# Performance work log

Measured on AMD Instinct MI355X. Metric: run time of the kernel, lower is better.

## Reference

```python
import math
import jax
import jax.numpy as jnp
import numpy as np

IMAGE_SIZE = 256
FOV_DEG = 60.0
NEAR, FAR = 0.01, 10.0
CHUNK = 128          # faces processed per scan step (bounds peak memory)
BIG_Z = 1e10         # 'infinite' depth for empty pixels


def _projection_matrix():
    f = 1.0 / math.tan(math.radians(FOV_DEG) / 2)
    return jnp.array([
        [f, 0.0, 0.0, 0.0],
        [0.0, f, 0.0, 0.0],
        [0.0, 0.0, (FAR + NEAR) / (NEAR - FAR), 2.0 * FAR * NEAR / (NEAR - FAR)],
        [0.0, 0.0, -1.0, 0.0],
    ], dtype=jnp.float32)


def _rasterize_mask(v_ndc, faces):
    """Coverage mask via edge-function triangle rasterization with a z-buffer.
    v_ndc: [V,3] ndc coords, faces: [F,3] int. Returns float [H,W] mask."""
    H = W = IMAGE_SIZE
    dt = v_ndc.dtype
    px = ((jnp.arange(W, dtype=dt) + 0.5) / W * 2.0 - 1.0)[None, None, :]  # [1,1,W]
    py = ((jnp.arange(H, dtype=dt) + 0.5) / H * 2.0 - 1.0)[None, :, None]  # [1,H,1]
    fchunks = faces.reshape(-1, CHUNK, 3)

    def body(carry, fc):
        zbuf, mask = carry
        tri = v_ndc[fc]  # [C,3,3]
        x0 = tri[:, 0, 0][:, None, None]; y0 = tri[:, 0, 1][:, None, None]; z0 = tri[:, 0, 2][:, None, None]
        x1 = tri[:, 1, 0][:, None, None]; y1 = tri[:, 1, 1][:, None, None]; z1 = tri[:, 1, 2][:, None, None]
        x2 = tri[:, 2, 0][:, None, None]; y2 = tri[:, 2, 1][:, None, None]; z2 = tri[:, 2, 2][:, None, None]
        # edge functions, [C,H,W]
        e0 = (x1 - x0) * (py - y0) - (y1 - y0) * (px - x0)
        e1 = (x2 - x1) * (py - y1) - (y2 - y1) * (px - x1)
        e2 = (x0 - x2) * (py - y2) - (y0 - y2) * (px - x2)
        inside = ((e0 >= 0) & (e1 >= 0) & (e2 >= 0)) | ((e0 <= 0) & (e1 <= 0) & (e2 <= 0))
        area = e0 + e1 + e2
        denom = jnp.where(jnp.abs(area) > 1e-12, area, 1.0)
        # barycentric-interpolated depth
        z = (e1 * z0 + e2 * z1 + e0 * z2) / denom
        zc = jnp.where(inside, z, BIG_Z)
        zbuf = jnp.minimum(zbuf, jnp.min(zc, axis=0))
        mask = jnp.maximum(mask, jnp.max(inside.astype(dt), axis=0))
        return (zbuf, mask), None

    zbuf0 = jnp.full((H, W), BIG_Z, dtype=dt)
    mask0 = jnp.zeros((H, W), dtype=dt)
    (_, mask), _ = jax.lax.scan(body, (zbuf0, mask0), fchunks)
    return mask


def setup_inputs() -> dict:
    key = jax.random.key(0)
    k1, k2, k3, k4 = jax.random.split(key, 4)
    B, V, F = 2, 4096, 4096
    verts = jax.random.normal(k1, (B, V, 3), dtype=jnp.float32)
    faces = jax.random.randint(k2, (B, F, 3), 0, V, dtype=jnp.int64 if jax.config.jax_enable_x64 else jnp.int32)
    R = jax.random.normal(k3, (B, 3, 3), dtype=jnp.float32)
    T = jax.random.normal(k4, (B, 3), dtype=jnp.float32)
    return {"verts": verts, "faces": faces, "R": R, "T": T}


def reference(verts, faces, R, T):
    proj = _projection_matrix()
    # world2cam: [R^T | -R^T t] with homogeneous bottom row, built batched
    Rt = jnp.swapaxes(R, -1, -2)                       # [B,3,3]
    t = -jnp.einsum('bij,bj->bi', Rt, T)               # [B,3]
    top = jnp.concatenate([Rt, t[..., None]], axis=-1)  # [B,3,4]
    bottom = jnp.broadcast_to(jnp.array([[0.0, 0.0, 0.0, 1.0]], dtype=verts.dtype), (R.shape[0], 1, 4))
    w2c = jnp.concatenate([top, bottom], axis=1)       # [B,4,4]
    VP = jnp.einsum('ij,bjk->bik', proj, w2c)          # [B,4,4]
    homo = jnp.concatenate([verts, jnp.ones_like(verts[..., :1])], axis=-1)  # [B,V,4]
    cam = jnp.einsum('bvk,bjk->bvj', homo, VP)         # verts_homo @ VP.T
    ndc = cam[..., :3] / jnp.maximum(cam[..., 3:], 1e-8)  # clamp(min=1e-8)
    mask = jax.vmap(_rasterize_mask)(ndc, faces)       # [B,H,W]
    return jnp.repeat(mask[..., None], 3, axis=-1)     # [B,H,W,3]
```

## Files before the change

### kernel.cpp

```cpp
#include <hip/hip_runtime.h>


#pragma clang fp contract(off)

#define HW      256
#define BATCH   2
#define VCOUNT  4096
#define FCOUNT  4096
#define CULL_EPS 1.52587890625e-05f

__global__ __launch_bounds__(256)
void face_pack_kernel(const float* __restrict__ verts,
                      const int* __restrict__ faces,
                      const float* __restrict__ R,
                      const float* __restrict__ T,
                      float4* __restrict__ fxy4,
                      float2* __restrict__ fxy2)
{
#pragma clang fp contract(off)
    int gid = blockIdx.x * blockDim.x + threadIdx.x;
    if (gid >= BATCH * FCOUNT) return;
    int b = gid / FCOUNT;

    const float fproj = 1.7320508075688772f;

    const float* Rb = R + b * 9;
    const float* Tb = T + b * 3;

    float t0 = -((Rb[0*3+0]*Tb[0] + Rb[1*3+0]*Tb[1]) + Rb[2*3+0]*Tb[2]);
    float t1 = -((Rb[0*3+1]*Tb[0] + Rb[1*3+1]*Tb[1]) + Rb[2*3+1]*Tb[2]);
    float t2 = -((Rb[0*3+2]*Tb[0] + Rb[1*3+2]*Tb[1]) + Rb[2*3+2]*Tb[2]);

    float VP00 = fproj * Rb[0*3+0], VP01 = fproj * Rb[1*3+0],
          VP02 = fproj * Rb[2*3+0], VP03 = fproj * t0;
    float VP10 = fproj * Rb[0*3+1], VP11 = fproj * Rb[1*3+1],
          VP12 = fproj * Rb[2*3+1], VP13 = fproj * t1;
    float VP30 = -Rb[0*3+2], VP31 = -Rb[1*3+2],
          VP32 = -Rb[2*3+2], VP33 = -t2;

    const int* fp = faces + (size_t)gid * 3;
    float xs[3], ys[3];
#pragma unroll
    for (int j = 0; j < 3; ++j) {
        const float* vv = verts + ((size_t)b * VCOUNT + fp[j]) * 3;
        float vx = vv[0], vy = vv[1], vz = vv[2];
        float cx = ((vx*VP00 + vy*VP01) + vz*VP02) + VP03;
        float cy = ((vx*VP10 + vy*VP11) + vz*VP12) + VP13;
        float cw = ((vx*VP30 + vy*VP31) + vz*VP32) + VP33;
        float w = fmaxf(cw, 1e-8f);
        xs[j] = cx / w;
        ys[j] = cy / w;
    }

    fxy4[gid] = make_float4(xs[0], ys[0], xs[1], ys[1]);
    fxy2[gid] = make_float2(xs[2], ys[2]);
}

__device__ __forceinline__ float bcast_lane(float v, int k) {
    return __int_as_float(__builtin_amdgcn_readlane(__float_as_int(v), k));
}

__global__ __launch_bounds__(256)
void raster_kernel(const float4* __restrict__ fxy4,
                   const float2* __restrict__ fxy2,
                   float* __restrict__ out)
{
#pragma clang fp contract(off)
    int b    = blockIdx.y;
    int tile = blockIdx.x;
    int tx = (tile & 15) << 4;
    int ty = (tile >> 4) << 4;

    int wave = threadIdx.x >> 6;
    int lane = threadIdx.x & 63;
    int qx = tx + ((wave & 1) << 3);
    int qy = ty + ((wave >> 1) << 3);
    int px_i = qx + (lane & 7);
    int py_i = qy + (lane >> 3);

    float px = (((float)px_i + 0.5f) / 256.0f) * 2.0f - 1.0f;
    float py = (((float)py_i + 0.5f) / 256.0f) * 2.0f - 1.0f;

    float pxlo = (((float)qx       + 0.5f) / 256.0f) * 2.0f - 1.0f;
    float pxhi = (((float)(qx + 7) + 0.5f) / 256.0f) * 2.0f - 1.0f;
    float pylo = (((float)qy       + 0.5f) / 256.0f) * 2.0f - 1.0f;
    float pyhi = (((float)(qy + 7) + 0.5f) / 256.0f) * 2.0f - 1.0f;

    const float4* f4 = fxy4 + (size_t)b * FCOUNT;
    const float2* f2 = fxy2 + (size_t)b * FCOUNT;

    bool covered = false;

    for (int g = 0; g < FCOUNT; g += 64) {
        if (__all((int)covered)) break;

        float4 q0 = f4[g + lane];
        float2 q1 = f2[g + lane];
        float x0 = q0.x, y0 = q0.y, x1 = q0.z, y1 = q0.w;
        float x2 = q1.x, y2 = q1.y;
        float d01x = x1 - x0, d01y = y1 - y0;
        float d12x = x2 - x1, d12y = y2 - y1;
        float d20x = x0 - x2, d20y = y0 - y2;

        bool killneg = false, killpos = false;
        {
            float A[3]  = { d01x, d12x, d20x };
            float Bc[3] = { -d01y, -d12y, -d20y };
            float xa[3] = { x0, x1, x2 };
            float ya[3] = { y0, y1, y2 };
#pragma unroll
            for (int e = 0; e < 3; ++e) {
                float C = (-Bc[e]) * xa[e] - A[e] * ya[e];
                float err = CULL_EPS * (fabsf(A[e])  * (1.0f + fabsf(ya[e]))
                                      + fabsf(Bc[e]) * (1.0f + fabsf(xa[e])));
                float yh = (A[e]  > 0.0f) ? pyhi : pylo;
                float yl = (A[e]  > 0.0f) ? pylo : pyhi;
                float xh = (Bc[e] > 0.0f) ? pxhi : pxlo;
                float xl = (Bc[e] > 0.0f) ? pxlo : pxhi;
                float hi = A[e] * yh + Bc[e] * xh + C;
                float lo = A[e] * yl + Bc[e] * xl + C;
                killneg = killneg || (hi < -err);
                killpos = killpos || (lo >  err);
            }
        }
        bool skip = killneg && killpos;

        unsigned long long m = __ballot((int)!skip);
        while (m) {
            if (__all((int)covered)) break;
            int k = __ffsll((long long)m) - 1;
            m &= m - 1;
            float bx0 = bcast_lane(x0, k), by0 = bcast_lane(y0, k);
            float bx1 = bcast_lane(x1, k), by1 = bcast_lane(y1, k);
            float bx2 = bcast_lane(x2, k), by2 = bcast_lane(y2, k);
            float bd01x = bcast_lane(d01x, k), bd01y = bcast_lane(d01y, k);
            float bd12x = bcast_lane(d12x, k), bd12y = bcast_lane(d12y, k);
            float bd20x = bcast_lane(d20x, k), bd20y = bcast_lane(d20y, k);
            float e0 = bd01x * (py - by0) - bd01y * (px - bx0);
            float e1 = bd12x * (py - by1) - bd12y * (px - bx1);
            float e2 = bd20x * (py - by2) - bd20y * (px - bx2);
            float mn = fminf(fminf(e0, e1), e2);
            float mx = fmaxf(fmaxf(e0, e1), e2);
            covered = covered || (mn >= 0.0f) || (mx <= 0.0f);
        }
    }

    float val = covered ? 1.0f : 0.0f;
    size_t o = ((size_t)(b * HW + py_i) * HW + px_i) * 3;
    out[o + 0] = val;
    out[o + 1] = val;
    out[o + 2] = val;
}

extern "C" void kernel_launch(void* const* d_in, const int* in_sizes, int n_in,
                              void* d_out, int out_size, void* d_ws, size_t ws_size,
                              hipStream_t stream) {
    const float* verts = (const float*)d_in[0];
    const int*   faces = (const int*)d_in[1];
    const float* R     = (const float*)d_in[2];
    const float* T     = (const float*)d_in[3];
    float*       out   = (float*)d_out;

    float4* fxy4 = (float4*)d_ws;
    float2* fxy2 = (float2*)(fxy4 + BATCH * FCOUNT);

    int nf = BATCH * FCOUNT;
    face_pack_kernel<<<(nf + 255) / 256, 256, 0, stream>>>(verts, faces, R, T,
                                                           fxy4, fxy2);

    dim3 grid(256, BATCH);
    raster_kernel<<<grid, 256, 0, stream>>>(fxy4, fxy2, out);
}
```

Measured before the change: 63.20 us.

## Precompute edge coefficients in pack kernel and use single-wave 8x8 tile blocks

The pack kernel now precomputes per-edge coefficients, constant terms and error bounds for each face. The raster kernel loads these and runs a center/radius tile-cull test with contraction enabled instead of rebuilding them per tile. Blocks shrink to one 64-lane wave per 8x8 tile, so the grid grows fourfold, and the per-triangle covered check inside the inner loop is dropped. The cost is extra global memory traffic for three float4 arrays per face, and the FMA contraction may change cull decisions near edges.

```diff
diff --git a/kernel.cpp b/kernel.cpp
--- a/kernel.cpp
+++ b/kernel.cpp
@@ -15,7 +15,10 @@
                       const float* __restrict__ R,
                       const float* __restrict__ T,
                       float4* __restrict__ fxy4,
-                      float2* __restrict__ fxy2)
+                      float2* __restrict__ fxy2,
+                      float4* __restrict__ ed0,
+                      float4* __restrict__ ed1,
+                      float4* __restrict__ ed2)
 {
 #pragma clang fp contract(off)
     int gid = blockIdx.x * blockDim.x + threadIdx.x;
@@ -54,27 +57,44 @@
 
     fxy4[gid] = make_float4(xs[0], ys[0], xs[1], ys[1]);
     fxy2[gid] = make_float2(xs[2], ys[2]);
+
+    float d01x = xs[1] - xs[0], d01y = ys[1] - ys[0];
+    float d12x = xs[2] - xs[1], d12y = ys[2] - ys[1];
+    float d20x = xs[0] - xs[2], d20y = ys[0] - ys[2];
+
+    float C0 = d01y * xs[0] - d01x * ys[0];
+    float C1 = d12y * xs[1] - d12x * ys[1];
+    float C2 = d20y * xs[2] - d20x * ys[2];
+    float e0r = CULL_EPS * (fabsf(d01x) * (1.0f + fabsf(ys[0]))
+                          + fabsf(d01y) * (1.0f + fabsf(xs[0])));
+    float e1r = CULL_EPS * (fabsf(d12x) * (1.0f + fabsf(ys[1]))
+                          + fabsf(d12y) * (1.0f + fabsf(xs[1])));
+    float e2r = CULL_EPS * (fabsf(d20x) * (1.0f + fabsf(ys[2]))
+                          + fabsf(d20y) * (1.0f + fabsf(xs[2])));
+
+    ed0[gid] = make_float4(d01x, -d01y, C0, e0r);
+    ed1[gid] = make_float4(d12x, -d12y, C1, e1r);
+    ed2[gid] = make_float4(d20x, -d20y, C2, e2r);
 }
 
 __device__ __forceinline__ float bcast_lane(float v, int k) {
     return __int_as_float(__builtin_amdgcn_readlane(__float_as_int(v), k));
 }
 
-__global__ __launch_bounds__(256)
-void raster_kernel(const float4* __restrict__ fxy4,
+__global__ __launch_bounds__(64)
+void raster_kernel(const float4* __restrict__ ed0,
+                   const float4* __restrict__ ed1,
+                   const float4* __restrict__ ed2,
+                   const float4* __restrict__ fxy4,
                    const float2* __restrict__ fxy2,
                    float* __restrict__ out)
 {
 #pragma clang fp contract(off)
     int b    = blockIdx.y;
     int tile = blockIdx.x;
-    int tx = (tile & 15) << 4;
-    int ty = (tile >> 4) << 4;
-
-    int wave = threadIdx.x >> 6;
-    int lane = threadIdx.x & 63;
-    int qx = tx + ((wave & 1) << 3);
-    int qy = ty + ((wave >> 1) << 3);
+    int qx = (tile & 31) << 3;
+    int qy = (tile >> 5) << 3;
+    int lane = threadIdx.x;
     int px_i = qx + (lane & 7);
     int py_i = qy + (lane >> 3);
 
@@ -85,60 +105,58 @@
     float pxhi = (((float)(qx + 7) + 0.5f) / 256.0f) * 2.0f - 1.0f;
     float pylo = (((float)qy       + 0.5f) / 256.0f) * 2.0f - 1.0f;
     float pyhi = (((float)(qy + 7) + 0.5f) / 256.0f) * 2.0f - 1.0f;
+    float xm = 0.5f * (pxlo + pxhi), xr = 0.5f * (pxhi - pxlo);
+    float ym = 0.5f * (pylo + pyhi), yr = 0.5f * (pyhi - pylo);
 
-    const float4* f4 = fxy4 + (size_t)b * FCOUNT;
-    const float2* f2 = fxy2 + (size_t)b * FCOUNT;
+    const float4* e0p = ed0  + (size_t)b * FCOUNT;
+    const float4* e1p = ed1  + (size_t)b * FCOUNT;
+    const float4* e2p = ed2  + (size_t)b * FCOUNT;
+    const float4* f4  = fxy4 + (size_t)b * FCOUNT;
+    const float2* f2  = fxy2 + (size_t)b * FCOUNT;
 
     bool covered = false;
 
     for (int g = 0; g < FCOUNT; g += 64) {
         if (__all((int)covered)) break;
 
-        float4 q0 = f4[g + lane];
-        float2 q1 = f2[g + lane];
-        float x0 = q0.x, y0 = q0.y, x1 = q0.z, y1 = q0.w;
-        float x2 = q1.x, y2 = q1.y;
-        float d01x = x1 - x0, d01y = y1 - y0;
-        float d12x = x2 - x1, d12y = y2 - y1;
-        float d20x = x0 - x2, d20y = y0 - y2;
+        int idx = g + lane;
+        float4 E0 = e0p[idx];
+        float4 E1 = e1p[idx];
+        float4 E2 = e2p[idx];
+        float4 q0 = f4[idx];
+        float2 q1 = f2[idx];
 
         bool killneg = false, killpos = false;
         {
-            float A[3]  = { d01x, d12x, d20x };
-            float Bc[3] = { -d01y, -d12y, -d20y };
-            float xa[3] = { x0, x1, x2 };
-            float ya[3] = { y0, y1, y2 };
-#pragma unroll
-            for (int e = 0; e < 3; ++e) {
-                float C = (-Bc[e]) * xa[e] - A[e] * ya[e];
-                float err = CULL_EPS * (fabsf(A[e])  * (1.0f + fabsf(ya[e]))
-                                      + fabsf(Bc[e]) * (1.0f + fabsf(xa[e])));
-                float yh = (A[e]  > 0.0f) ? pyhi : pylo;
-                float yl = (A[e]  > 0.0f) ? pylo : pyhi;
-                float xh = (Bc[e] > 0.0f) ? pxhi : pxlo;
-                float xl = (Bc[e] > 0.0f) ? pxlo : pxhi;
-                float hi = A[e] * yh + Bc[e] * xh + C;
-                float lo = A[e] * yl + Bc[e] * xl + C;
-                killneg = killneg || (hi < -err);
-                killpos = killpos || (lo >  err);
-            }
+#pragma clang fp contract(fast)
+            float b0 = E0.x * ym + E0.y * xm + E0.z;
+            float s0 = fabsf(E0.x) * yr + fabsf(E0.y) * xr;
+            killneg = killneg || (b0 + s0 < -E0.w);
+            killpos = killpos || (b0 - s0 >  E0.w);
+            float b1 = E1.x * ym + E1.y * xm + E1.z;
+            float s1 = fabsf(E1.x) * yr + fabsf(E1.y) * xr;
+            killneg = killneg || (b1 + s1 < -E1.w);
+            killpos = killpos || (b1 - s1 >  E1.w);
+            float b2 = E2.x * ym + E2.y * xm + E2.z;
+            float s2 = fabsf(E2.x) * yr + fabsf(E2.y) * xr;
+            killneg = killneg || (b2 + s2 < -E2.w);
+            killpos = killpos || (b2 - s2 >  E2.w);
         }
         bool skip = killneg && killpos;
 
         unsigned long long m = __ballot((int)!skip);
         while (m) {
-            if (__all((int)covered)) break;
             int k = __ffsll((long long)m) - 1;
             m &= m - 1;
-            float bx0 = bcast_lane(x0, k), by0 = bcast_lane(y0, k);
-            float bx1 = bcast_lane(x1, k), by1 = bcast_lane(y1, k);
-            float bx2 = bcast_lane(x2, k), by2 = bcast_lane(y2, k);
-            float bd01x = bcast_lane(d01x, k), bd01y = bcast_lane(d01y, k);
-            float bd12x = bcast_lane(d12x, k), bd12y = bcast_lane(d12y, k);
-            float bd20x = bcast_lane(d20x, k), bd20y = bcast_lane(d20y, k);
-            float e0 = bd01x * (py - by0) - bd01y * (px - bx0);
-            float e1 = bd12x * (py - by1) - bd12y * (px - bx1);
-            float e2 = bd20x * (py - by2) - bd20y * (px - bx2);
+            float A0 = bcast_lane(E0.x, k), B0 = bcast_lane(E0.y, k);
+            float A1 = bcast_lane(E1.x, k), B1 = bcast_lane(E1.y, k);
+            float A2 = bcast_lane(E2.x, k), B2 = bcast_lane(E2.y, k);
+            float ax0 = bcast_lane(q0.x, k), ay0 = bcast_lane(q0.y, k);
+            float ax1 = bcast_lane(q0.z, k), ay1 = bcast_lane(q0.w, k);
+            float ax2 = bcast_lane(q1.x, k), ay2 = bcast_lane(q1.y, k);
+            float e0 = A0 * (py - ay0) + B0 * (px - ax0);
+            float e1 = A1 * (py - ay1) + B1 * (px - ax1);
+            float e2 = A2 * (py - ay2) + B2 * (px - ax2);
             float mn = fminf(fminf(e0, e1), e2);
             float mx = fmaxf(fmaxf(e0, e1), e2);
             covered = covered || (mn >= 0.0f) || (mx <= 0.0f);
@@ -163,11 +181,15 @@
 
     float4* fxy4 = (float4*)d_ws;
     float2* fxy2 = (float2*)(fxy4 + BATCH * FCOUNT);
+    float4* ed0  = (float4*)(fxy2 + BATCH * FCOUNT);
+    float4* ed1  = ed0 + BATCH * FCOUNT;
+    float4* ed2  = ed1 + BATCH * FCOUNT;
 
     int nf = BATCH * FCOUNT;
     face_pack_kernel<<<(nf + 255) / 256, 256, 0, stream>>>(verts, faces, R, T,
-                                                           fxy4, fxy2);
+                                                           fxy4, fxy2,
+                                                           ed0, ed1, ed2);
 
-    dim3 grid(256, BATCH);
-    raster_kernel<<<grid, 256, 0, stream>>>(fxy4, fxy2, out);
+    dim3 grid(32 * 32, BATCH);
+    raster_kernel<<<grid, 64, 0, stream>>>(ed0, ed1, ed2, fxy4, fxy2, out);
 }
```

Result: no change. 63.92 us (+1.1%).

## Fuse face projection into raster kernel with per-block LDS face cache

Applied to the files above, without the earlier changes.

Merges the face-packing and rasterization kernels into one launch. Each 512-thread block projects all faces for its batch into shared memory (96 KB) and then rasterizes eight independent 8x8 tiles from LDS instead of from global memory. It also recomputes edge deltas from broadcast vertices rather than broadcasting them, and drops the per-face early-exit check in the inner loop. The cost is that projection work is repeated in every block (128 blocks per batch), and the large LDS footprint limits occupancy.

```diff
diff --git a/kernel.cpp b/kernel.cpp
--- a/kernel.cpp
+++ b/kernel.cpp
@@ -7,23 +7,28 @@
 #define BATCH   2
 #define VCOUNT  4096
 #define FCOUNT  4096
+#define WAVES   8
 #define CULL_EPS 1.52587890625e-05f
 
-__global__ __launch_bounds__(256)
-void face_pack_kernel(const float* __restrict__ verts,
-                      const int* __restrict__ faces,
-                      const float* __restrict__ R,
-                      const float* __restrict__ T,
-                      float4* __restrict__ fxy4,
-                      float2* __restrict__ fxy2)
+__device__ __forceinline__ float bcast_lane(float v, int k) {
+    return __int_as_float(__builtin_amdgcn_readlane(__float_as_int(v), k));
+}
+
+__global__ __launch_bounds__(64 * WAVES)
+void render_kernel(const float* __restrict__ verts,
+                   const int* __restrict__ faces,
+                   const float* __restrict__ R,
+                   const float* __restrict__ T,
+                   float* __restrict__ out)
 {
 #pragma clang fp contract(off)
-    int gid = blockIdx.x * blockDim.x + threadIdx.x;
-    if (gid >= BATCH * FCOUNT) return;
-    int b = gid / FCOUNT;
+    __shared__ float4 sA[FCOUNT];
+    __shared__ float2 sB[FCOUNT];
+
+    int b   = blockIdx.y;
+    int tid = threadIdx.x;
 
     const float fproj = 1.7320508075688772f;
-
     const float* Rb = R + b * 9;
     const float* Tb = T + b * 3;
 
@@ -38,43 +43,30 @@
     float VP30 = -Rb[0*3+2], VP31 = -Rb[1*3+2],
           VP32 = -Rb[2*3+2], VP33 = -t2;
 
-    const int* fp = faces + (size_t)gid * 3;
-    float xs[3], ys[3];
+    for (int f = tid; f < FCOUNT; f += 64 * WAVES) {
+        const int* fp = faces + ((size_t)b * FCOUNT + f) * 3;
+        float xs[3], ys[3];
 #pragma unroll
-    for (int j = 0; j < 3; ++j) {
-        const float* vv = verts + ((size_t)b * VCOUNT + fp[j]) * 3;
-        float vx = vv[0], vy = vv[1], vz = vv[2];
-        float cx = ((vx*VP00 + vy*VP01) + vz*VP02) + VP03;
-        float cy = ((vx*VP10 + vy*VP11) + vz*VP12) + VP13;
-        float cw = ((vx*VP30 + vy*VP31) + vz*VP32) + VP33;
-        float w = fmaxf(cw, 1e-8f);
-        xs[j] = cx / w;
-        ys[j] = cy / w;
+        for (int j = 0; j < 3; ++j) {
+            const float* vv = verts + ((size_t)b * VCOUNT + fp[j]) * 3;
+            float vx = vv[0], vy = vv[1], vz = vv[2];
+            float cx = ((vx*VP00 + vy*VP01) + vz*VP02) + VP03;
+            float cy = ((vx*VP10 + vy*VP11) + vz*VP12) + VP13;
+            float cw = ((vx*VP30 + vy*VP31) + vz*VP32) + VP33;
+            float w = fmaxf(cw, 1e-8f);
+            xs[j] = cx / w;
+            ys[j] = cy / w;
+        }
+        sA[f] = make_float4(xs[0], ys[0], xs[1], ys[1]);
+        sB[f] = make_float2(xs[2], ys[2]);
     }
+    __syncthreads();
 
-    fxy4[gid] = make_float4(xs[0], ys[0], xs[1], ys[1]);
-    fxy2[gid] = make_float2(xs[2], ys[2]);
-}
-
-__device__ __forceinline__ float bcast_lane(float v, int k) {
-    return __int_as_float(__builtin_amdgcn_readlane(__float_as_int(v), k));
-}
-
-__global__ __launch_bounds__(256)
-void raster_kernel(const float4* __restrict__ fxy4,
-                   const float2* __restrict__ fxy2,
-                   float* __restrict__ out)
-{
-#pragma clang fp contract(off)
-    int b    = blockIdx.y;
-    int tile = blockIdx.x;
-    int tx = (tile & 15) << 4;
-    int ty = (tile >> 4) << 4;
-
-    int wave = threadIdx.x >> 6;
-    int lane = threadIdx.x & 63;
-    int qx = tx + ((wave & 1) << 3);
-    int qy = ty + ((wave >> 1) << 3);
+    int wave = tid >> 6;
+    int lane = tid & 63;
+    int tile = blockIdx.x * WAVES + wave;
+    int qx = (tile & 31) << 3;
+    int qy = (tile >> 5) << 3;
     int px_i = qx + (lane & 7);
     int py_i = qy + (lane >> 3);
 
@@ -86,16 +78,13 @@
     float pylo = (((float)qy       + 0.5f) / 256.0f) * 2.0f - 1.0f;
     float pyhi = (((float)(qy + 7) + 0.5f) / 256.0f) * 2.0f - 1.0f;
 
-    const float4* f4 = fxy4 + (size_t)b * FCOUNT;
-    const float2* f2 = fxy2 + (size_t)b * FCOUNT;
-
     bool covered = false;
 
     for (int g = 0; g < FCOUNT; g += 64) {
         if (__all((int)covered)) break;
 
-        float4 q0 = f4[g + lane];
-        float2 q1 = f2[g + lane];
+        float4 q0 = sA[g + lane];
+        float2 q1 = sB[g + lane];
         float x0 = q0.x, y0 = q0.y, x1 = q0.z, y1 = q0.w;
         float x2 = q1.x, y2 = q1.y;
         float d01x = x1 - x0, d01y = y1 - y0;
@@ -127,15 +116,14 @@
 
         unsigned long long m = __ballot((int)!skip);
         while (m) {
-            if (__all((int)covered)) break;
             int k = __ffsll((long long)m) - 1;
             m &= m - 1;
             float bx0 = bcast_lane(x0, k), by0 = bcast_lane(y0, k);
             float bx1 = bcast_lane(x1, k), by1 = bcast_lane(y1, k);
             float bx2 = bcast_lane(x2, k), by2 = bcast_lane(y2, k);
-            float bd01x = bcast_lane(d01x, k), bd01y = bcast_lane(d01y, k);
-            float bd12x = bcast_lane(d12x, k), bd12y = bcast_lane(d12y, k);
-            float bd20x = bcast_lane(d20x, k), bd20y = bcast_lane(d20y, k);
+            float bd01x = bx1 - bx0, bd01y = by1 - by0;
+            float bd12x = bx2 - bx1, bd12y = by2 - by1;
+            float bd20x = bx0 - bx2, bd20y = by0 - by2;
             float e0 = bd01x * (py - by0) - bd01y * (px - bx0);
             float e1 = bd12x * (py - by1) - bd12y * (px - bx1);
             float e2 = bd20x * (py - by2) - bd20y * (px - bx2);
@@ -161,13 +149,8 @@
     const float* T     = (const float*)d_in[3];
     float*       out   = (float*)d_out;
 
-    float4* fxy4 = (float4*)d_ws;
-    float2* fxy2 = (float2*)(fxy4 + BATCH * FCOUNT);
+    (void)d_ws; (void)ws_size;
 
-    int nf = BATCH * FCOUNT;
-    face_pack_kernel<<<(nf + 255) / 256, 256, 0, stream>>>(verts, faces, R, T,
-                                                           fxy4, fxy2);
-
-    dim3 grid(256, BATCH);
-    raster_kernel<<<grid, 256, 0, stream>>>(fxy4, fxy2, out);
+    dim3 grid(1024 / WAVES, BATCH);
+    render_kernel<<<grid, 64 * WAVES, 0, stream>>>(verts, faces, R, T, out);
 }
```

Measured after the change: 69.03 us. 1.09x slower.
